# Kernel optimization log

Measured on AMD Instinct MI355X. Metric: run time of the kernel, lower is better.

Reference implementation:

```python
import jax, jax.numpy as jnp
import numpy as np

N, E, F, H, C = 100000, 1600000, 128, 128, 64

def setup_inputs() -> dict:
    key = jax.random.key(0)
    ks = jax.random.split(key, 16)
    def u(k, shape, fan_out):
        s = 1.0 / np.sqrt(fan_out)
        return jax.random.uniform(k, shape, jnp.float32, -s, s)
    return {
        'x': jax.random.normal(ks[0], (N, F), jnp.float32),
        'edge_index': jax.random.randint(ks[1], (2, E), 0, N, jnp.int32),
        # layer 1: F -> H  (stdv = 1/sqrt(out_features); att vecs stdv=1; att_vec stdv=1/sqrt(3))
        'W_low1': u(ks[2], (F, H), H), 'W_high1': u(ks[3], (F, H), H), 'W_mlp1': u(ks[4], (F, H), H),
        'v_low1': u(ks[5], (H, 1), 1), 'v_high1': u(ks[6], (H, 1), 1), 'v_mlp1': u(ks[7], (H, 1), 1),
        'att1': u(ks[8], (3, 3), 3),
        # layer 2: H -> C
        'W_low2': u(ks[9], (H, C), C), 'W_high2': u(ks[10], (H, C), C), 'W_mlp2': u(ks[11], (H, C), C),
        'v_low2': u(ks[12], (C, 1), 1), 'v_high2': u(ks[13], (C, 1), 1), 'v_mlp2': u(ks[14], (C, 1), 1),
        'att2': u(ks[15], (3, 3), 3),
    }

def reference(x, edge_index, W_low1, W_high1, W_mlp1, v_low1, v_high1, v_mlp1, att1,
              W_low2, W_high2, W_mlp2, v_low2, v_high2, v_mlp2, att2):
    row, col = edge_index[0], edge_index[1]
    # row-normalized adjacency: adj_low[i,j] = 1/deg(i); deg==0 rows -> zero output
    deg = jax.ops.segment_sum(jnp.ones((E,), x.dtype), row, num_segments=N)
    inv_deg = jnp.where(deg > 0, 1.0 / jnp.maximum(deg, 1.0), 0.0)[:, None]  # [N,1]

    def spmm_low(h):  # adj_low @ h
        return inv_deg * jax.ops.segment_sum(h[col], row, num_segments=N)

    T = 3.0
    def acm_layer(h, Wl, Wh, Wm, vl, vh, vm, av):
        hl = h @ Wl
        hh = h @ Wh
        out_low = jax.nn.relu(spmm_low(hl))
        out_high = jax.nn.relu(hh - spmm_low(hh))  # adj_high = I - adj_low
        out_mlp = jax.nn.relu(h @ Wm)
        logits = jnp.concatenate([out_low @ vl, out_high @ vh, out_mlp @ vm], axis=1)  # [N,3]
        att = jax.nn.softmax((jax.nn.sigmoid(logits) @ av) / T, axis=1)  # [N,3]
        return 3.0 * (att[:, 0:1] * out_low + att[:, 1:2] * out_high + att[:, 2:3] * out_mlp)

    fea = acm_layer(x, W_low1, W_high1, W_mlp1, v_low1, v_high1, v_mlp1, att1)
    fea = jax.nn.relu(fea)  # dropout is identity at eval
    return acm_layer(fea, W_low2, W_high2, W_mlp2, v_low2, v_high2, v_mlp2, att2)
```

## Files before the change

kernel.cpp:

```cpp
#include <hip/hip_runtime.h>

typedef unsigned short u16;
typedef unsigned int u32;
typedef unsigned long long u64;
typedef __attribute__((ext_vector_type(8))) short short8;
typedef __attribute__((ext_vector_type(4))) float f32x4;
typedef __attribute__((ext_vector_type(4))) u32 u32x4;

#define BSHIFT 8
#define MAXBUCK 512
#define BCAP 8192

__device__ __forceinline__ float bf2f(u32 u) {
    union { u32 i; float f; } v; v.i = u << 16; return v.f;
}
__device__ __forceinline__ float bf2fh(u32 u) {
    union { u32 i; float f; } v; v.i = u & 0xffff0000u; return v.f;
}
__device__ __forceinline__ u16 f2bf(float f) {
    union { float f; u32 i; } v; v.f = f;
    u32 u = (v.i + 0x7fffu + ((v.i >> 16) & 1u)) >> 16;
    return (u16)u;
}

__device__ __forceinline__ int swz(int ci) { return ci ^ ((ci >> 4) & 7); }

__device__ __forceinline__ int xcd_swz(int bid, int nbg) {
    int q = nbg >> 3, r = nbg & 7;
    int x = bid & 7, i = bid >> 3;
    return (x < r) ? (x * (q + 1) + i) : (r * (q + 1) + (x - r) * q + i);
}

#define CASTBLK 2048
__global__ void k_prep(const float4* __restrict__ X, u32* __restrict__ Xb, long total4,
                       const float* __restrict__ Wl1, const float* __restrict__ Wh1,
                       const float* __restrict__ Wm1, const float* __restrict__ Wl2,
                       const float* __restrict__ Wh2, const float* __restrict__ Wm2,
                       u16* __restrict__ Wp1, u16* __restrict__ Wp2) {
    if (blockIdx.x < CASTBLK) {
        long i = (long)blockIdx.x * blockDim.x + threadIdx.x;
        long stride = (long)CASTBLK * blockDim.x;
        for (; i < total4; i += stride) {
            float4 p = X[i];
            Xb[i * 2 + 0] = (u32)f2bf(p.x) | ((u32)f2bf(p.y) << 16);
            Xb[i * 2 + 1] = (u32)f2bf(p.z) | ((u32)f2bf(p.w) << 16);
        }
        return;
    }
    int tid = (blockIdx.x - CASTBLK) * blockDim.x + threadIdx.x;
    int nthr = 16 * blockDim.x;
    for (int m = 0; m < 8; ++m) {
        int layer = m >> 2;
        int slot = m & 3;
        int Hout = layer ? 64 : 128;
        const float* W = layer ? (slot == 0 ? Wl2 : (slot == 3 ? Wm2 : Wh2))
                               : (slot == 0 ? Wl1 : (slot == 3 ? Wm1 : Wh1));
        float sgn = (slot == 1) ? -1.f : 1.f;
        u16* dst = (layer ? Wp2 : Wp1) + slot * Hout * 128;
        int total = 128 * Hout;
        for (int i = tid; i < total; i += nthr) {
            int T = i / 2048;
            int c = (i / 512) & 3;
            int lane = (i / 8) & 63;
            int j = i & 7;
            int col = T * 16 + (lane & 15);
            int k = c * 32 + (lane >> 4) * 8 + j;
            dst[i] = f2bf(sgn * W[k * Hout + col]);
        }
    }
}

__global__ void k_bscatter_f(const int* __restrict__ erow, const int* __restrict__ ecol, int e,
                             int nbuck, int* __restrict__ gcursor, u32* __restrict__ bedge) {
    __shared__ int hist[MAXBUCK];
    __shared__ int base[MAXBUCK];
    for (int t = threadIdx.x; t < nbuck; t += blockDim.x) hist[t] = 0;
    __syncthreads();
    int chunk = (e + gridDim.x - 1) / gridDim.x;
    int lo = blockIdx.x * chunk, hi = min(e, lo + chunk);
    for (int i = lo + threadIdx.x; i < hi; i += blockDim.x)
        atomicAdd(&hist[erow[i] >> BSHIFT], 1);
    __syncthreads();
    for (int t = threadIdx.x; t < nbuck; t += blockDim.x) {
        int c = hist[t];
        base[t] = c ? atomicAdd(&gcursor[t], c) : 0;
        hist[t] = 0;
    }
    __syncthreads();
    for (int i = lo + threadIdx.x; i < hi; i += blockDim.x) {
        int r = erow[i];
        int bk = r >> BSHIFT;
        int pos = base[bk] + atomicAdd(&hist[bk], 1);
        if (pos < BCAP)
            bedge[(size_t)bk * BCAP + pos] = ((u32)ecol[i] << 8) | (u32)(r & 255);
    }
}

__global__ void k_bscan2(const int* __restrict__ bcnt, int nbuck, int* __restrict__ boff) {
    __shared__ int lds[MAXBUCK];
    int t = threadIdx.x;
    int v = (t < nbuck) ? bcnt[t] : 0;
    lds[t] = v; __syncthreads();
    for (int off = 1; off < MAXBUCK; off <<= 1) {
        int x = (t >= off) ? lds[t - off] : 0;
        __syncthreads();
        lds[t] += x;
        __syncthreads();
    }
    if (t < nbuck) {
        boff[t] = lds[t] - v;
        if (t == nbuck - 1) boff[nbuck] = lds[t];
    }
}

__global__ void k_bfill2f(const u32* __restrict__ bedge, const int* __restrict__ bcnt,
                          const int* __restrict__ boff, int n,
                          int* __restrict__ row_ptr, float* __restrict__ inv_deg,
                          int* __restrict__ cols) {
    __shared__ int cnt[256];
    __shared__ int incl[256];
    __shared__ int pos[256];
    int b = blockIdx.x, t = threadIdx.x;
    cnt[t] = 0;
    __syncthreads();
    int rbase = b << BSHIFT;
    const u32* src = bedge + (size_t)b * BCAP;
    int cb = bcnt[b];
    int lo = boff[b];
    for (int i = t; i < cb; i += 256)
        atomicAdd(&cnt[src[i] & 255u], 1);
    __syncthreads();
    int v = cnt[t];
    incl[t] = v;
    __syncthreads();
    for (int off = 1; off < 256; off <<= 1) {
        int x = (t >= off) ? incl[t - off] : 0;
        __syncthreads();
        incl[t] += x;
        __syncthreads();
    }
    int excl = incl[t] - v;
    pos[t] = excl;
    int row = rbase + t;
    if (row < n) {
        row_ptr[row] = lo + excl;
        inv_deg[row] = v > 0 ? 1.f / (float)v : 0.f;
    }
    if (b == (int)gridDim.x - 1 && t == 0) row_ptr[n] = lo + cb;
    __syncthreads();
    for (int i = t; i < cb; i += 256) {
        u32 vv = src[i];
        int rl = (int)(vv & 255u);
        int p = lo + atomicAdd(&pos[rl], 1);
        cols[p] = (int)(vv >> 8);
    }
}

template<int HOUT, bool L1>
__global__ __launch_bounds__(256, 4)
void k_fused(const u32* __restrict__ X2, const int* __restrict__ row_ptr,
             const int* __restrict__ cols, const float* __restrict__ inv_deg,
             const u16* __restrict__ Wp,
             const float* __restrict__ vl, const float* __restrict__ vh, const float* __restrict__ vm,
             const float* __restrict__ att, int n,
             u16* __restrict__ feaOut, float* __restrict__ fOut) {
    constexpr int KPG = HOUT / 64;
    constexpr int NTw = 3 * KPG;
    constexpr int ROWS = 16;
    __shared__ __align__(16) u32 AsU[1024];
    __shared__ __align__(16) u32 AxU[1024];
    __shared__ int rctr;
    int w = threadIdx.x >> 6, lane = threadIdx.x & 63;
    int ql = lane & 15;
    int ln15 = lane & 15, lq = lane >> 4;
    int tile = xcd_swz(blockIdx.x, gridDim.x);
    int m0 = tile * ROWS;
    const u32x4* X16 = (const u32x4*)X2;

    if (threadIdx.x == 0) rctr = 0;
    __syncthreads();

    for (;;) {
        int rv;
        if (ql == 0) rv = atomicAdd(&rctr, 1);
        rv = __shfl(rv, 0, 16);
        if (rv >= ROWS) break;
        int row = m0 + rv;
        int beg = 0, end = 0;
        float s = 0.f;
        u32x4 px = {0u, 0u, 0u, 0u};
        if (row < n) {
            beg = row_ptr[row];
            end = row_ptr[row + 1];
            s = inv_deg[row];
            px = X16[(size_t)row * 16 + ql];
        }
        float a0 = 0.f, a1 = 0.f, a2 = 0.f, a3 = 0.f, a4 = 0.f, a5 = 0.f, a6 = 0.f, a7 = 0.f;
        int myc = (beg + ql < end) ? cols[beg + ql] : 0;
        for (int j0 = beg; j0 < end; j0 += 16) {
            int cnt = end - j0; if (cnt > 16) cnt = 16;
            int nmy = (j0 + 16 + ql < end) ? cols[j0 + 16 + ql] : 0;
            int j = 0;
            for (; j + 8 <= cnt; j += 8) {
                int c0 = __shfl(myc, j + 0, 16);
                int c1 = __shfl(myc, j + 1, 16);
                int c2 = __shfl(myc, j + 2, 16);
                int c3 = __shfl(myc, j + 3, 16);
                int c4 = __shfl(myc, j + 4, 16);
                int c5 = __shfl(myc, j + 5, 16);
                int c6 = __shfl(myc, j + 6, 16);
                int c7 = __shfl(myc, j + 7, 16);
                u32x4 p0 = X16[(size_t)c0 * 16 + ql];
                u32x4 p1 = X16[(size_t)c1 * 16 + ql];
                u32x4 p2 = X16[(size_t)c2 * 16 + ql];
                u32x4 p3 = X16[(size_t)c3 * 16 + ql];
                u32x4 p4 = X16[(size_t)c4 * 16 + ql];
                u32x4 p5 = X16[(size_t)c5 * 16 + ql];
                u32x4 p6 = X16[(size_t)c6 * 16 + ql];
                u32x4 p7 = X16[(size_t)c7 * 16 + ql];
                a0 += bf2f(p0[0] & 0xffffu) + bf2f(p1[0] & 0xffffu) + bf2f(p2[0] & 0xffffu) + bf2f(p3[0] & 0xffffu)
                    + bf2f(p4[0] & 0xffffu) + bf2f(p5[0] & 0xffffu) + bf2f(p6[0] & 0xffffu) + bf2f(p7[0] & 0xffffu);
                a1 += bf2fh(p0[0]) + bf2fh(p1[0]) + bf2fh(p2[0]) + bf2fh(p3[0])
                    + bf2fh(p4[0]) + bf2fh(p5[0]) + bf2fh(p6[0]) + bf2fh(p7[0]);
                a2 += bf2f(p0[1] & 0xffffu) + bf2f(p1[1] & 0xffffu) + bf2f(p2[1] & 0xffffu) + bf2f(p3[1] & 0xffffu)
                    + bf2f(p4[1] & 0xffffu) + bf2f(p5[1] & 0xffffu) + bf2f(p6[1] & 0xffffu) + bf2f(p7[1] & 0xffffu);
                a3 += bf2fh(p0[1]) + bf2fh(p1[1]) + bf2fh(p2[1]) + bf2fh(p3[1])
                    + bf2fh(p4[1]) + bf2fh(p5[1]) + bf2fh(p6[1]) + bf2fh(p7[1]);
                a4 += bf2f(p0[2] & 0xffffu) + bf2f(p1[2] & 0xffffu) + bf2f(p2[2] & 0xffffu) + bf2f(p3[2] & 0xffffu)
                    + bf2f(p4[2] & 0xffffu) + bf2f(p5[2] & 0xffffu) + bf2f(p6[2] & 0xffffu) + bf2f(p7[2] & 0xffffu);
                a5 += bf2fh(p0[2]) + bf2fh(p1[2]) + bf2fh(p2[2]) + bf2fh(p3[2])
                    + bf2fh(p4[2]) + bf2fh(p5[2]) + bf2fh(p6[2]) + bf2fh(p7[2]);
                a6 += bf2f(p0[3] & 0xffffu) + bf2f(p1[3] & 0xffffu) + bf2f(p2[3] & 0xffffu) + bf2f(p3[3] & 0xffffu)
                    + bf2f(p4[3] & 0xffffu) + bf2f(p5[3] & 0xffffu) + bf2f(p6[3] & 0xffffu) + bf2f(p7[3] & 0xffffu);
                a7 += bf2fh(p0[3]) + bf2fh(p1[3]) + bf2fh(p2[3]) + bf2fh(p3[3])
                    + bf2fh(p4[3]) + bf2fh(p5[3]) + bf2fh(p6[3]) + bf2fh(p7[3]);
            }
            for (; j + 4 <= cnt; j += 4) {
                int c0 = __shfl(myc, j + 0, 16);
                int c1 = __shfl(myc, j + 1, 16);
                int c2 = __shfl(myc, j + 2, 16);
                int c3 = __shfl(myc, j + 3, 16);
                u32x4 p0 = X16[(size_t)c0 * 16 + ql];
                u32x4 p1 = X16[(size_t)c1 * 16 + ql];
                u32x4 p2 = X16[(size_t)c2 * 16 + ql];
                u32x4 p3 = X16[(size_t)c3 * 16 + ql];
                a0 += bf2f(p0[0] & 0xffffu) + bf2f(p1[0] & 0xffffu) + bf2f(p2[0] & 0xffffu) + bf2f(p3[0] & 0xffffu);
                a1 += bf2fh(p0[0]) + bf2fh(p1[0]) + bf2fh(p2[0]) + bf2fh(p3[0]);
                a2 += bf2f(p0[1] & 0xffffu) + bf2f(p1[1] & 0xffffu) + bf2f(p2[1] & 0xffffu) + bf2f(p3[1] & 0xffffu);
                a3 += bf2fh(p0[1]) + bf2fh(p1[1]) + bf2fh(p2[1]) + bf2fh(p3[1]);
                a4 += bf2f(p0[2] & 0xffffu) + bf2f(p1[2] & 0xffffu) + bf2f(p2[2] & 0xffffu) + bf2f(p3[2] & 0xffffu);
                a5 += bf2fh(p0[2]) + bf2fh(p1[2]) + bf2fh(p2[2]) + bf2fh(p3[2]);
                a6 += bf2f(p0[3] & 0xffffu) + bf2f(p1[3] & 0xffffu) + bf2f(p2[3] & 0xffffu) + bf2f(p3[3] & 0xffffu);
                a7 += bf2fh(p0[3]) + bf2fh(p1[3]) + bf2fh(p2[3]) + bf2fh(p3[3]);
            }
            for (; j < cnt; ++j) {
                int c = __shfl(myc, j, 16);
                u32x4 p = X16[(size_t)c * 16 + ql];
                a0 += bf2f(p[0] & 0xffffu);
                a1 += bf2fh(p[0]);
                a2 += bf2f(p[1] & 0xffffu);
                a3 += bf2fh(p[1]);
                a4 += bf2f(p[2] & 0xffffu);
                a5 += bf2fh(p[2]);
                a6 += bf2f(p[3] & 0xffffu);
                a7 += bf2fh(p[3]);
            }
            myc = nmy;
        }
        int ci = (ql >> 2) * 64 + (ql & 3) * 16 + rv;
        int d = swz(ci) * 4;
        u32x4 sv;
        sv[0] = (u32)f2bf(a0 * s) | ((u32)f2bf(a1 * s) << 16);
        sv[1] = (u32)f2bf(a2 * s) | ((u32)f2bf(a3 * s) << 16);
        sv[2] = (u32)f2bf(a4 * s) | ((u32)f2bf(a5 * s) << 16);
        sv[3] = (u32)f2bf(a6 * s) | ((u32)f2bf(a7 * s) << 16);
        *(u32x4*)(AsU + d) = sv;
        *(u32x4*)(AxU + d) = px;
    }

    f32x4 acc[NTw];
#pragma unroll
    for (int k = 0; k < NTw; ++k) { f32x4 z = {0.f, 0.f, 0.f, 0.f}; acc[k] = z; }

    __syncthreads();

    const u16* As = (const u16*)AsU;
    const u16* Ax = (const u16*)AxU;
#pragma unroll
    for (int c = 0; c < 4; ++c) {
        int ci = c * 64 + lane;
        int o = swz(ci) * 8;
        short8 as = *(const short8*)(As + o);
        short8 ax = *(const short8*)(Ax + o);
#pragma unroll
        for (int kk = 0; kk < KPG; ++kk) {
            int T = w + kk * 4;
            size_t fo = (size_t)(T * 4 + c) * 512 + lane * 8;
            short8 bl  = *(const short8*)(Wp + (size_t)0 * (HOUT * 128) + fo);
            short8 bhn = *(const short8*)(Wp + (size_t)1 * (HOUT * 128) + fo);
            short8 bhp = *(const short8*)(Wp + (size_t)2 * (HOUT * 128) + fo);
            short8 bm  = *(const short8*)(Wp + (size_t)3 * (HOUT * 128) + fo);
            acc[0 * KPG + kk] = __builtin_amdgcn_mfma_f32_16x16x32_bf16(as, bl,  acc[0 * KPG + kk], 0, 0, 0);
            acc[1 * KPG + kk] = __builtin_amdgcn_mfma_f32_16x16x32_bf16(as, bhn, acc[1 * KPG + kk], 0, 0, 0);
            acc[1 * KPG + kk] = __builtin_amdgcn_mfma_f32_16x16x32_bf16(ax, bhp, acc[1 * KPG + kk], 0, 0, 0);
            acc[2 * KPG + kk] = __builtin_amdgcn_mfma_f32_16x16x32_bf16(ax, bm,  acc[2 * KPG + kk], 0, 0, 0);
        }
    }

    float vval[NTw];
#pragma unroll
    for (int k = 0; k < NTw; ++k) {
        int g = k / KPG, kk = k % KPG;
        int col = w * 16 + kk * 64 + ln15;
        vval[k] = (g == 0 ? vl : (g == 1 ? vh : vm))[col];
    }

    __shared__ float part[4][3][ROWS];
    __shared__ float wgt[ROWS][3];
    {
        float pdg[3][4];
#pragma unroll
        for (int g = 0; g < 3; ++g)
#pragma unroll
            for (int r = 0; r < 4; ++r) pdg[g][r] = 0.f;
#pragma unroll
        for (int k = 0; k < NTw; ++k) {
            int g = k / KPG;
#pragma unroll
            for (int r = 0; r < 4; ++r)
                pdg[g][r] += fmaxf(acc[k][r], 0.f) * vval[k];
        }
#pragma unroll
        for (int off = 1; off < 16; off <<= 1)
#pragma unroll
            for (int g = 0; g < 3; ++g)
#pragma unroll
                for (int r = 0; r < 4; ++r)
                    pdg[g][r] += __shfl_xor(pdg[g][r], off);
        if (ln15 == 0) {
            int rbase = lq * 4;
#pragma unroll
            for (int g = 0; g < 3; ++g)
#pragma unroll
                for (int r = 0; r < 4; ++r)
                    part[w][g][rbase + r] = pdg[g][r];
        }
    }
    __syncthreads();
    if (threadIdx.x < ROWS) {
        int row = threadIdx.x;
        float d0 = 0.f, d1 = 0.f, d2 = 0.f;
#pragma unroll
        for (int q = 0; q < 4; ++q) {
            d0 += part[q][0][row];
            d1 += part[q][1][row];
            d2 += part[q][2][row];
        }
        float s0 = 1.f / (1.f + __expf(-d0));
        float s1 = 1.f / (1.f + __expf(-d1));
        float s2 = 1.f / (1.f + __expf(-d2));
        float a0 = (s0 * att[0] + s1 * att[3] + s2 * att[6]) * (1.f / 3.f);
        float a1 = (s0 * att[1] + s1 * att[4] + s2 * att[7]) * (1.f / 3.f);
        float a2 = (s0 * att[2] + s1 * att[5] + s2 * att[8]) * (1.f / 3.f);
        float mx = fmaxf(a0, fmaxf(a1, a2));
        float e0 = __expf(a0 - mx), e1 = __expf(a1 - mx), e2 = __expf(a2 - mx);
        float inv = 3.f / (e0 + e1 + e2);
        wgt[row][0] = e0 * inv;
        wgt[row][1] = e1 * inv;
        wgt[row][2] = e2 * inv;
    }
    __syncthreads();

#pragma unroll
    for (int kk = 0; kk < KPG; ++kk)
#pragma unroll
        for (int r = 0; r < 4; ++r) {
            int row_local = lq * 4 + r;
            int row = m0 + row_local;
            if (row < n) {
                int col = w * 16 + kk * 64 + ln15;
                float w0 = wgt[row_local][0], w1 = wgt[row_local][1], w2 = wgt[row_local][2];
                float ol = fmaxf(acc[0 * KPG + kk][r], 0.f);
                float oh = fmaxf(acc[1 * KPG + kk][r], 0.f);
                float om = fmaxf(acc[2 * KPG + kk][r], 0.f);
                float val = w0 * ol + w1 * oh + w2 * om;
                if (L1)
                    feaOut[(size_t)row * HOUT + col] = f2bf(fmaxf(val, 0.f));
                else
                    fOut[(size_t)row * HOUT + col] = val;
            }
        }
}

extern "C" void kernel_launch(void* const* d_in, const int* in_sizes, int n_in,
                              void* d_out, int out_size, void* d_ws, size_t ws_size,
                              hipStream_t stream) {
    const int F = 128;
    int n = in_sizes[0] / F;
    int e = in_sizes[1] / 2;
    int nbuck = (n + (1 << BSHIFT) - 1) >> BSHIFT;
    const float* x = (const float*)d_in[0];
    const int* ei = (const int*)d_in[1];
    const int* erow = ei;
    const int* ecol = ei + e;
    const float *Wl1 = (const float*)d_in[2], *Wh1 = (const float*)d_in[3], *Wm1 = (const float*)d_in[4];
    const float *vl1 = (const float*)d_in[5], *vh1 = (const float*)d_in[6], *vm1 = (const float*)d_in[7];
    const float* att1 = (const float*)d_in[8];
    const float *Wl2 = (const float*)d_in[9], *Wh2 = (const float*)d_in[10], *Wm2 = (const float*)d_in[11];
    const float *vl2 = (const float*)d_in[12], *vh2 = (const float*)d_in[13], *vm2 = (const float*)d_in[14];
    const float* att2 = (const float*)d_in[15];
    float* out = (float*)d_out;

    char* ws = (char*)d_ws;
    size_t off = 0;
    auto alloc = [&](size_t b) -> void* {
        void* p = ws + off;
        off = (off + b + 255) & ~(size_t)255;
        return p;
    };
    int* row_ptr = (int*)alloc((size_t)(n + 1) * 4);
    float* inv_deg = (float*)alloc((size_t)n * 4);
    int* gcursor = (int*)alloc(MAXBUCK * 4);
    int* boff = (int*)alloc((MAXBUCK + 1) * 4);
    u32* bedge = (u32*)alloc((size_t)MAXBUCK * BCAP * 4);
    int* cols = (int*)alloc((size_t)e * 4);
    u16* Xb = (u16*)alloc((size_t)n * 128 * 2);
    u16* fea = (u16*)alloc((size_t)n * 128 * 2);
    u16* Wp1 = (u16*)alloc((size_t)4 * 128 * 128 * 2);
    u16* Wp2 = (u16*)alloc((size_t)4 * 64 * 128 * 2);
    (void)ws_size; (void)n_in; (void)out_size;

    k_prep<<<CASTBLK + 16, 256, 0, stream>>>((const float4*)x, (u32*)Xb, (long)n * 32,
                                             Wl1, Wh1, Wm1, Wl2, Wh2, Wm2, Wp1, Wp2);

    hipMemsetAsync(gcursor, 0, (size_t)MAXBUCK * 4, stream);
    k_bscatter_f<<<256, 256, 0, stream>>>(erow, ecol, e, nbuck, gcursor, bedge);
    k_bscan2<<<1, MAXBUCK, 0, stream>>>(gcursor, nbuck, boff);
    k_bfill2f<<<nbuck, 256, 0, stream>>>(bedge, gcursor, boff, n, row_ptr, inv_deg, cols);

    int gb = (n + 15) / 16;

    k_fused<128, true><<<gb, 256, 0, stream>>>((const u32*)Xb, row_ptr, cols, inv_deg,
                                               Wp1, vl1, vh1, vm1, att1, n, fea, nullptr);
    k_fused<64, false><<<gb, 256, 0, stream>>>((const u32*)fea, row_ptr, cols, inv_deg,
                                               Wp2, vl2, vh2, vm2, att2, n, nullptr, out);
}
```

Measured before the change: 339.6 us.

## Make fused GNN layers persistent with atomic tile queue and merge prep kernels

The fused layer kernels become persistent: a capped grid of blocks pulls 16-row tiles from a global atomic counter instead of launching one block per tile with XCD swizzling. Attention parameters and v-vectors are hoisted out of the tile loop. Launch bounds rise to 6 blocks per CU. The input cast/weight-pack kernel and the edge bucket scatter kernel are merged into one launch. The aim is to cut launch and tail overhead and balance irregular row degrees, at the cost of per-tile atomics, extra barriers, the loss of XCD locality and more register pressure.

```diff
diff --git a/kernel.cpp b/kernel.cpp
--- a/kernel.cpp
+++ b/kernel.cpp
@@ -10,6 +10,8 @@
 #define BSHIFT 8
 #define MAXBUCK 512
 #define BCAP 8192
+#define CASTBLK 2048
+#define SCATBLK 256
 
 __device__ __forceinline__ float bf2f(u32 u) {
     union { u32 i; float f; } v; v.i = u << 16; return v.f;
@@ -25,18 +27,15 @@
 
 __device__ __forceinline__ int swz(int ci) { return ci ^ ((ci >> 4) & 7); }
 
-__device__ __forceinline__ int xcd_swz(int bid, int nbg) {
-    int q = nbg >> 3, r = nbg & 7;
-    int x = bid & 7, i = bid >> 3;
-    return (x < r) ? (x * (q + 1) + i) : (r * (q + 1) + (x - r) * q + i);
-}
-
-#define CASTBLK 2048
-__global__ void k_prep(const float4* __restrict__ X, u32* __restrict__ Xb, long total4,
-                       const float* __restrict__ Wl1, const float* __restrict__ Wh1,
-                       const float* __restrict__ Wm1, const float* __restrict__ Wl2,
-                       const float* __restrict__ Wh2, const float* __restrict__ Wm2,
-                       u16* __restrict__ Wp1, u16* __restrict__ Wp2) {
+__global__ void k_prep_scat(const float4* __restrict__ X, u32* __restrict__ Xb, long total4,
+                            const float* __restrict__ Wl1, const float* __restrict__ Wh1,
+                            const float* __restrict__ Wm1, const float* __restrict__ Wl2,
+                            const float* __restrict__ Wh2, const float* __restrict__ Wm2,
+                            u16* __restrict__ Wp1, u16* __restrict__ Wp2,
+                            const int* __restrict__ erow, const int* __restrict__ ecol, int e,
+                            int nbuck, int* __restrict__ gcursor, u32* __restrict__ bedge) {
+    __shared__ int hist[MAXBUCK];
+    __shared__ int base[MAXBUCK];
     if (blockIdx.x < CASTBLK) {
         long i = (long)blockIdx.x * blockDim.x + threadIdx.x;
         long stride = (long)CASTBLK * blockDim.x;
@@ -47,37 +46,35 @@
         }
         return;
     }
-    int tid = (blockIdx.x - CASTBLK) * blockDim.x + threadIdx.x;
-    int nthr = 16 * blockDim.x;
-    for (int m = 0; m < 8; ++m) {
-        int layer = m >> 2;
-        int slot = m & 3;
-        int Hout = layer ? 64 : 128;
-        const float* W = layer ? (slot == 0 ? Wl2 : (slot == 3 ? Wm2 : Wh2))
-                               : (slot == 0 ? Wl1 : (slot == 3 ? Wm1 : Wh1));
-        float sgn = (slot == 1) ? -1.f : 1.f;
-        u16* dst = (layer ? Wp2 : Wp1) + slot * Hout * 128;
-        int total = 128 * Hout;
-        for (int i = tid; i < total; i += nthr) {
-            int T = i / 2048;
-            int c = (i / 512) & 3;
-            int lane = (i / 8) & 63;
-            int j = i & 7;
-            int col = T * 16 + (lane & 15);
-            int k = c * 32 + (lane >> 4) * 8 + j;
-            dst[i] = f2bf(sgn * W[k * Hout + col]);
-        }
-    }
-}
-
-__global__ void k_bscatter_f(const int* __restrict__ erow, const int* __restrict__ ecol, int e,
-                             int nbuck, int* __restrict__ gcursor, u32* __restrict__ bedge) {
-    __shared__ int hist[MAXBUCK];
-    __shared__ int base[MAXBUCK];
+    if (blockIdx.x < CASTBLK + 16) {
+        int tid = (blockIdx.x - CASTBLK) * blockDim.x + threadIdx.x;
+        int nthr = 16 * blockDim.x;
+        for (int m = 0; m < 8; ++m) {
+            int layer = m >> 2;
+            int slot = m & 3;
+            int Hout = layer ? 64 : 128;
+            const float* W = layer ? (slot == 0 ? Wl2 : (slot == 3 ? Wm2 : Wh2))
+                                   : (slot == 0 ? Wl1 : (slot == 3 ? Wm1 : Wh1));
+            float sgn = (slot == 1) ? -1.f : 1.f;
+            u16* dst = (layer ? Wp2 : Wp1) + slot * Hout * 128;
+            int total = 128 * Hout;
+            for (int i = tid; i < total; i += nthr) {
+                int T = i / 2048;
+                int c = (i / 512) & 3;
+                int lane = (i / 8) & 63;
+                int j = i & 7;
+                int col = T * 16 + (lane & 15);
+                int k = c * 32 + (lane >> 4) * 8 + j;
+                dst[i] = f2bf(sgn * W[k * Hout + col]);
+            }
+        }
+        return;
+    }
+    int bid = blockIdx.x - (CASTBLK + 16);
     for (int t = threadIdx.x; t < nbuck; t += blockDim.x) hist[t] = 0;
     __syncthreads();
-    int chunk = (e + gridDim.x - 1) / gridDim.x;
-    int lo = blockIdx.x * chunk, hi = min(e, lo + chunk);
+    int chunk = (e + SCATBLK - 1) / SCATBLK;
+    int lo = bid * chunk, hi = min(e, lo + chunk);
     for (int i = lo + threadIdx.x; i < hi; i += blockDim.x)
         atomicAdd(&hist[erow[i] >> BSHIFT], 1);
     __syncthreads();
@@ -157,155 +154,26 @@
 }
 
 template<int HOUT, bool L1>
-__global__ __launch_bounds__(256, 4)
+__global__ __launch_bounds__(256, 6)
 void k_fused(const u32* __restrict__ X2, const int* __restrict__ row_ptr,
              const int* __restrict__ cols, const float* __restrict__ inv_deg,
              const u16* __restrict__ Wp,
              const float* __restrict__ vl, const float* __restrict__ vh, const float* __restrict__ vm,
-             const float* __restrict__ att, int n,
+             const float* __restrict__ att, int n, int ntiles, int* __restrict__ gctr,
              u16* __restrict__ feaOut, float* __restrict__ fOut) {
     constexpr int KPG = HOUT / 64;
     constexpr int NTw = 3 * KPG;
     constexpr int ROWS = 16;
     __shared__ __align__(16) u32 AsU[1024];
     __shared__ __align__(16) u32 AxU[1024];
+    __shared__ float part[4][3][ROWS];
+    __shared__ float wgt[ROWS][3];
+    __shared__ int tshare;
     __shared__ int rctr;
     int w = threadIdx.x >> 6, lane = threadIdx.x & 63;
     int ql = lane & 15;
     int ln15 = lane & 15, lq = lane >> 4;
-    int tile = xcd_swz(blockIdx.x, gridDim.x);
-    int m0 = tile * ROWS;
     const u32x4* X16 = (const u32x4*)X2;
-
-    if (threadIdx.x == 0) rctr = 0;
-    __syncthreads();
-
-    for (;;) {
-        int rv;
-        if (ql == 0) rv = atomicAdd(&rctr, 1);
-        rv = __shfl(rv, 0, 16);
-        if (rv >= ROWS) break;
-        int row = m0 + rv;
-        int beg = 0, end = 0;
-        float s = 0.f;
-        u32x4 px = {0u, 0u, 0u, 0u};
-        if (row < n) {
-            beg = row_ptr[row];
-            end = row_ptr[row + 1];
-            s = inv_deg[row];
-            px = X16[(size_t)row * 16 + ql];
-        }
-        float a0 = 0.f, a1 = 0.f, a2 = 0.f, a3 = 0.f, a4 = 0.f, a5 = 0.f, a6 = 0.f, a7 = 0.f;
-        int myc = (beg + ql < end) ? cols[beg + ql] : 0;
-        for (int j0 = beg; j0 < end; j0 += 16) {
-            int cnt = end - j0; if (cnt > 16) cnt = 16;
-            int nmy = (j0 + 16 + ql < end) ? cols[j0 + 16 + ql] : 0;
-            int j = 0;
-            for (; j + 8 <= cnt; j += 8) {
-                int c0 = __shfl(myc, j + 0, 16);
-                int c1 = __shfl(myc, j + 1, 16);
-                int c2 = __shfl(myc, j + 2, 16);
-                int c3 = __shfl(myc, j + 3, 16);
-                int c4 = __shfl(myc, j + 4, 16);
-                int c5 = __shfl(myc, j + 5, 16);
-                int c6 = __shfl(myc, j + 6, 16);
-                int c7 = __shfl(myc, j + 7, 16);
-                u32x4 p0 = X16[(size_t)c0 * 16 + ql];
-                u32x4 p1 = X16[(size_t)c1 * 16 + ql];
-                u32x4 p2 = X16[(size_t)c2 * 16 + ql];
-                u32x4 p3 = X16[(size_t)c3 * 16 + ql];
-                u32x4 p4 = X16[(size_t)c4 * 16 + ql];
-                u32x4 p5 = X16[(size_t)c5 * 16 + ql];
-                u32x4 p6 = X16[(size_t)c6 * 16 + ql];
-                u32x4 p7 = X16[(size_t)c7 * 16 + ql];
-                a0 += bf2f(p0[0] & 0xffffu) + bf2f(p1[0] & 0xffffu) + bf2f(p2[0] & 0xffffu) + bf2f(p3[0] & 0xffffu)
-                    + bf2f(p4[0] & 0xffffu) + bf2f(p5[0] & 0xffffu) + bf2f(p6[0] & 0xffffu) + bf2f(p7[0] & 0xffffu);
-                a1 += bf2fh(p0[0]) + bf2fh(p1[0]) + bf2fh(p2[0]) + bf2fh(p3[0])
-                    + bf2fh(p4[0]) + bf2fh(p5[0]) + bf2fh(p6[0]) + bf2fh(p7[0]);
-                a2 += bf2f(p0[1] & 0xffffu) + bf2f(p1[1] & 0xffffu) + bf2f(p2[1] & 0xffffu) + bf2f(p3[1] & 0xffffu)
-                    + bf2f(p4[1] & 0xffffu) + bf2f(p5[1] & 0xffffu) + bf2f(p6[1] & 0xffffu) + bf2f(p7[1] & 0xffffu);
-                a3 += bf2fh(p0[1]) + bf2fh(p1[1]) + bf2fh(p2[1]) + bf2fh(p3[1])
-                    + bf2fh(p4[1]) + bf2fh(p5[1]) + bf2fh(p6[1]) + bf2fh(p7[1]);
-                a4 += bf2f(p0[2] & 0xffffu) + bf2f(p1[2] & 0xffffu) + bf2f(p2[2] & 0xffffu) + bf2f(p3[2] & 0xffffu)
-                    + bf2f(p4[2] & 0xffffu) + bf2f(p5[2] & 0xffffu) + bf2f(p6[2] & 0xffffu) + bf2f(p7[2] & 0xffffu);
-                a5 += bf2fh(p0[2]) + bf2fh(p1[2]) + bf2fh(p2[2]) + bf2fh(p3[2])
-                    + bf2fh(p4[2]) + bf2fh(p5[2]) + bf2fh(p6[2]) + bf2fh(p7[2]);
-                a6 += bf2f(p0[3] & 0xffffu) + bf2f(p1[3] & 0xffffu) + bf2f(p2[3] & 0xffffu) + bf2f(p3[3] & 0xffffu)
-                    + bf2f(p4[3] & 0xffffu) + bf2f(p5[3] & 0xffffu) + bf2f(p6[3] & 0xffffu) + bf2f(p7[3] & 0xffffu);
-                a7 += bf2fh(p0[3]) + bf2fh(p1[3]) + bf2fh(p2[3]) + bf2fh(p3[3])
-                    + bf2fh(p4[3]) + bf2fh(p5[3]) + bf2fh(p6[3]) + bf2fh(p7[3]);
-            }
-            for (; j + 4 <= cnt; j += 4) {
-                int c0 = __shfl(myc, j + 0, 16);
-                int c1 = __shfl(myc, j + 1, 16);
-                int c2 = __shfl(myc, j + 2, 16);
-                int c3 = __shfl(myc, j + 3, 16);
-                u32x4 p0 = X16[(size_t)c0 * 16 + ql];
-                u32x4 p1 = X16[(size_t)c1 * 16 + ql];
-                u32x4 p2 = X16[(size_t)c2 * 16 + ql];
-                u32x4 p3 = X16[(size_t)c3 * 16 + ql];
-                a0 += bf2f(p0[0] & 0xffffu) + bf2f(p1[0] & 0xffffu) + bf2f(p2[0] & 0xffffu) + bf2f(p3[0] & 0xffffu);
-                a1 += bf2fh(p0[0]) + bf2fh(p1[0]) + bf2fh(p2[0]) + bf2fh(p3[0]);
-                a2 += bf2f(p0[1] & 0xffffu) + bf2f(p1[1] & 0xffffu) + bf2f(p2[1] & 0xffffu) + bf2f(p3[1] & 0xffffu);
-                a3 += bf2fh(p0[1]) + bf2fh(p1[1]) + bf2fh(p2[1]) + bf2fh(p3[1]);
-                a4 += bf2f(p0[2] & 0xffffu) + bf2f(p1[2] & 0xffffu) + bf2f(p2[2] & 0xffffu) + bf2f(p3[2] & 0xffffu);
-                a5 += bf2fh(p0[2]) + bf2fh(p1[2]) + bf2fh(p2[2]) + bf2fh(p3[2]);
-                a6 += bf2f(p0[3] & 0xffffu) + bf2f(p1[3] & 0xffffu) + bf2f(p2[3] & 0xffffu) + bf2f(p3[3] & 0xffffu);
-                a7 += bf2fh(p0[3]) + bf2fh(p1[3]) + bf2fh(p2[3]) + bf2fh(p3[3]);
-            }
-            for (; j < cnt; ++j) {
-                int c = __shfl(myc, j, 16);
-                u32x4 p = X16[(size_t)c * 16 + ql];
-                a0 += bf2f(p[0] & 0xffffu);
-                a1 += bf2fh(p[0]);
-                a2 += bf2f(p[1] & 0xffffu);
-                a3 += bf2fh(p[1]);
-                a4 += bf2f(p[2] & 0xffffu);
-                a5 += bf2fh(p[2]);
-                a6 += bf2f(p[3] & 0xffffu);
-                a7 += bf2fh(p[3]);
-            }
-            myc = nmy;
-        }
-        int ci = (ql >> 2) * 64 + (ql & 3) * 16 + rv;
-        int d = swz(ci) * 4;
-        u32x4 sv;
-        sv[0] = (u32)f2bf(a0 * s) | ((u32)f2bf(a1 * s) << 16);
-        sv[1] = (u32)f2bf(a2 * s) | ((u32)f2bf(a3 * s) << 16);
-        sv[2] = (u32)f2bf(a4 * s) | ((u32)f2bf(a5 * s) << 16);
-        sv[3] = (u32)f2bf(a6 * s) | ((u32)f2bf(a7 * s) << 16);
-        *(u32x4*)(AsU + d) = sv;
-        *(u32x4*)(AxU + d) = px;
-    }
-
-    f32x4 acc[NTw];
-#pragma unroll
-    for (int k = 0; k < NTw; ++k) { f32x4 z = {0.f, 0.f, 0.f, 0.f}; acc[k] = z; }
-
-    __syncthreads();
-
-    const u16* As = (const u16*)AsU;
-    const u16* Ax = (const u16*)AxU;
-#pragma unroll
-    for (int c = 0; c < 4; ++c) {
-        int ci = c * 64 + lane;
-        int o = swz(ci) * 8;
-        short8 as = *(const short8*)(As + o);
-        short8 ax = *(const short8*)(Ax + o);
-#pragma unroll
-        for (int kk = 0; kk < KPG; ++kk) {
-            int T = w + kk * 4;
-            size_t fo = (size_t)(T * 4 + c) * 512 + lane * 8;
-            short8 bl  = *(const short8*)(Wp + (size_t)0 * (HOUT * 128) + fo);
-            short8 bhn = *(const short8*)(Wp + (size_t)1 * (HOUT * 128) + fo);
-            short8 bhp = *(const short8*)(Wp + (size_t)2 * (HOUT * 128) + fo);
-            short8 bm  = *(const short8*)(Wp + (size_t)3 * (HOUT * 128) + fo);
-            acc[0 * KPG + kk] = __builtin_amdgcn_mfma_f32_16x16x32_bf16(as, bl,  acc[0 * KPG + kk], 0, 0, 0);
-            acc[1 * KPG + kk] = __builtin_amdgcn_mfma_f32_16x16x32_bf16(as, bhn, acc[1 * KPG + kk], 0, 0, 0);
-            acc[1 * KPG + kk] = __builtin_amdgcn_mfma_f32_16x16x32_bf16(ax, bhp, acc[1 * KPG + kk], 0, 0, 0);
-            acc[2 * KPG + kk] = __builtin_amdgcn_mfma_f32_16x16x32_bf16(ax, bm,  acc[2 * KPG + kk], 0, 0, 0);
-        }
-    }
 
     float vval[NTw];
 #pragma unroll
@@ -314,82 +182,221 @@
         int col = w * 16 + kk * 64 + ln15;
         vval[k] = (g == 0 ? vl : (g == 1 ? vh : vm))[col];
     }
-
-    __shared__ float part[4][3][ROWS];
-    __shared__ float wgt[ROWS][3];
-    {
-        float pdg[3][4];
-#pragma unroll
-        for (int g = 0; g < 3; ++g)
-#pragma unroll
-            for (int r = 0; r < 4; ++r) pdg[g][r] = 0.f;
-#pragma unroll
-        for (int k = 0; k < NTw; ++k) {
-            int g = k / KPG;
-#pragma unroll
-            for (int r = 0; r < 4; ++r)
-                pdg[g][r] += fmaxf(acc[k][r], 0.f) * vval[k];
-        }
-#pragma unroll
-        for (int off = 1; off < 16; off <<= 1)
+    float at0 = att[0], at1 = att[1], at2 = att[2], at3 = att[3], at4 = att[4];
+    float at5 = att[5], at6 = att[6], at7 = att[7], at8 = att[8];
+
+    for (;;) {
+        if (threadIdx.x == 0) {
+            tshare = atomicAdd(gctr, 1);
+            rctr = 0;
+        }
+        __syncthreads();
+        int tile = tshare;
+        if (tile >= ntiles) break;
+        int m0 = tile * ROWS;
+
+        for (;;) {
+            int rv;
+            if (ql == 0) rv = atomicAdd(&rctr, 1);
+            rv = __shfl(rv, 0, 16);
+            if (rv >= ROWS) break;
+            int row = m0 + rv;
+            int beg = 0, end = 0;
+            float s = 0.f;
+            u32x4 px = {0u, 0u, 0u, 0u};
+            if (row < n) {
+                beg = row_ptr[row];
+                end = row_ptr[row + 1];
+                s = inv_deg[row];
+                px = X16[(size_t)row * 16 + ql];
+            }
+            float a0 = 0.f, a1 = 0.f, a2 = 0.f, a3 = 0.f, a4 = 0.f, a5 = 0.f, a6 = 0.f, a7 = 0.f;
+            int myc = (beg + ql < end) ? cols[beg + ql] : 0;
+            for (int j0 = beg; j0 < end; j0 += 16) {
+                int cnt = end - j0; if (cnt > 16) cnt = 16;
+                int nmy = (j0 + 16 + ql < end) ? cols[j0 + 16 + ql] : 0;
+                int j = 0;
+                for (; j + 8 <= cnt; j += 8) {
+                    int c0 = __shfl(myc, j + 0, 16);
+                    int c1 = __shfl(myc, j + 1, 16);
+                    int c2 = __shfl(myc, j + 2, 16);
+                    int c3 = __shfl(myc, j + 3, 16);
+                    int c4 = __shfl(myc, j + 4, 16);
+                    int c5 = __shfl(myc, j + 5, 16);
+                    int c6 = __shfl(myc, j + 6, 16);
+                    int c7 = __shfl(myc, j + 7, 16);
+                    u32x4 p0 = X16[(size_t)c0 * 16 + ql];
+                    u32x4 p1 = X16[(size_t)c1 * 16 + ql];
+                    u32x4 p2 = X16[(size_t)c2 * 16 + ql];
+                    u32x4 p3 = X16[(size_t)c3 * 16 + ql];
+                    u32x4 p4 = X16[(size_t)c4 * 16 + ql];
+                    u32x4 p5 = X16[(size_t)c5 * 16 + ql];
+                    u32x4 p6 = X16[(size_t)c6 * 16 + ql];
+                    u32x4 p7 = X16[(size_t)c7 * 16 + ql];
+                    a0 += bf2f(p0[0] & 0xffffu) + bf2f(p1[0] & 0xffffu) + bf2f(p2[0] & 0xffffu) + bf2f(p3[0] & 0xffffu)
+                        + bf2f(p4[0] & 0xffffu) + bf2f(p5[0] & 0xffffu) + bf2f(p6[0] & 0xffffu) + bf2f(p7[0] & 0xffffu);
+                    a1 += bf2fh(p0[0]) + bf2fh(p1[0]) + bf2fh(p2[0]) + bf2fh(p3[0])
+                        + bf2fh(p4[0]) + bf2fh(p5[0]) + bf2fh(p6[0]) + bf2fh(p7[0]);
+                    a2 += bf2f(p0[1] & 0xffffu) + bf2f(p1[1] & 0xffffu) + bf2f(p2[1] & 0xffffu) + bf2f(p3[1] & 0xffffu)
+                        + bf2f(p4[1] & 0xffffu) + bf2f(p5[1] & 0xffffu) + bf2f(p6[1] & 0xffffu) + bf2f(p7[1] & 0xffffu);
+                    a3 += bf2fh(p0[1]) + bf2fh(p1[1]) + bf2fh(p2[1]) + bf2fh(p3[1])
+                        + bf2fh(p4[1]) + bf2fh(p5[1]) + bf2fh(p6[1]) + bf2fh(p7[1]);
+                    a4 += bf2f(p0[2] & 0xffffu) + bf2f(p1[2] & 0xffffu) + bf2f(p2[2] & 0xffffu) + bf2f(p3[2] & 0xffffu)
+                        + bf2f(p4[2] & 0xffffu) + bf2f(p5[2] & 0xffffu) + bf2f(p6[2] & 0xffffu) + bf2f(p7[2] & 0xffffu);
+                    a5 += bf2fh(p0[2]) + bf2fh(p1[2]) + bf2fh(p2[2]) + bf2fh(p3[2])
+                        + bf2fh(p4[2]) + bf2fh(p5[2]) + bf2fh(p6[2]) + bf2fh(p7[2]);
+                    a6 += bf2f(p0[3] & 0xffffu) + bf2f(p1[3] & 0xffffu) + bf2f(p2[3] & 0xffffu) + bf2f(p3[3] & 0xffffu)
+                        + bf2f(p4[3] & 0xffffu) + bf2f(p5[3] & 0xffffu) + bf2f(p6[3] & 0xffffu) + bf2f(p7[3] & 0xffffu);
+                    a7 += bf2fh(p0[3]) + bf2fh(p1[3]) + bf2fh(p2[3]) + bf2fh(p3[3])
+                        + bf2fh(p4[3]) + bf2fh(p5[3]) + bf2fh(p6[3]) + bf2fh(p7[3]);
+                }
+                for (; j + 4 <= cnt; j += 4) {
+                    int c0 = __shfl(myc, j + 0, 16);
+                    int c1 = __shfl(myc, j + 1, 16);
+                    int c2 = __shfl(myc, j + 2, 16);
+                    int c3 = __shfl(myc, j + 3, 16);
+                    u32x4 p0 = X16[(size_t)c0 * 16 + ql];
+                    u32x4 p1 = X16[(size_t)c1 * 16 + ql];
+                    u32x4 p2 = X16[(size_t)c2 * 16 + ql];
+                    u32x4 p3 = X16[(size_t)c3 * 16 + ql];
+                    a0 += bf2f(p0[0] & 0xffffu) + bf2f(p1[0] & 0xffffu) + bf2f(p2[0] & 0xffffu) + bf2f(p3[0] & 0xffffu);
+                    a1 += bf2fh(p0[0]) + bf2fh(p1[0]) + bf2fh(p2[0]) + bf2fh(p3[0]);
+                    a2 += bf2f(p0[1] & 0xffffu) + bf2f(p1[1] & 0xffffu) + bf2f(p2[1] & 0xffffu) + bf2f(p3[1] & 0xffffu);
+                    a3 += bf2fh(p0[1]) + bf2fh(p1[1]) + bf2fh(p2[1]) + bf2fh(p3[1]);
+                    a4 += bf2f(p0[2] & 0xffffu) + bf2f(p1[2] & 0xffffu) + bf2f(p2[2] & 0xffffu) + bf2f(p3[2] & 0xffffu);
+                    a5 += bf2fh(p0[2]) + bf2fh(p1[2]) + bf2fh(p2[2]) + bf2fh(p3[2]);
+                    a6 += bf2f(p0[3] & 0xffffu) + bf2f(p1[3] & 0xffffu) + bf2f(p2[3] & 0xffffu) + bf2f(p3[3] & 0xffffu);
+                    a7 += bf2fh(p0[3]) + bf2fh(p1[3]) + bf2fh(p2[3]) + bf2fh(p3[3]);
+                }
+                for (; j < cnt; ++j) {
+                    int c = __shfl(myc, j, 16);
+                    u32x4 p = X16[(size_t)c * 16 + ql];
+                    a0 += bf2f(p[0] & 0xffffu);
+                    a1 += bf2fh(p[0]);
+                    a2 += bf2f(p[1] & 0xffffu);
+                    a3 += bf2fh(p[1]);
+                    a4 += bf2f(p[2] & 0xffffu);
+                    a5 += bf2fh(p[2]);
+                    a6 += bf2f(p[3] & 0xffffu);
+                    a7 += bf2fh(p[3]);
+                }
+                myc = nmy;
+            }
+            int ci = (ql >> 2) * 64 + (ql & 3) * 16 + rv;
+            int d = swz(ci) * 4;
+            u32x4 sv;
+            sv[0] = (u32)f2bf(a0 * s) | ((u32)f2bf(a1 * s) << 16);
+            sv[1] = (u32)f2bf(a2 * s) | ((u32)f2bf(a3 * s) << 16);
+            sv[2] = (u32)f2bf(a4 * s) | ((u32)f2bf(a5 * s) << 16);
+            sv[3] = (u32)f2bf(a6 * s) | ((u32)f2bf(a7 * s) << 16);
+            *(u32x4*)(AsU + d) = sv;
+            *(u32x4*)(AxU + d) = px;
+        }
+
+        f32x4 acc[NTw];
+#pragma unroll
+        for (int k = 0; k < NTw; ++k) { f32x4 z = {0.f, 0.f, 0.f, 0.f}; acc[k] = z; }
+
+        __syncthreads();
+
+        const u16* As = (const u16*)AsU;
+        const u16* Ax = (const u16*)AxU;
+#pragma unroll
+        for (int c = 0; c < 4; ++c) {
+            int ci = c * 64 + lane;
+            int o = swz(ci) * 8;
+            short8 as = *(const short8*)(As + o);
+            short8 ax = *(const short8*)(Ax + o);
+#pragma unroll
+            for (int kk = 0; kk < KPG; ++kk) {
+                int T = w + kk * 4;
+                size_t fo = (size_t)(T * 4 + c) * 512 + lane * 8;
+                short8 bl  = *(const short8*)(Wp + (size_t)0 * (HOUT * 128) + fo);
+                short8 bhn = *(const short8*)(Wp + (size_t)1 * (HOUT * 128) + fo);
+                short8 bhp = *(const short8*)(Wp + (size_t)2 * (HOUT * 128) + fo);
+                short8 bm  = *(const short8*)(Wp + (size_t)3 * (HOUT * 128) + fo);
+                acc[0 * KPG + kk] = __builtin_amdgcn_mfma_f32_16x16x32_bf16(as, bl,  acc[0 * KPG + kk], 0, 0, 0);
+                acc[1 * KPG + kk] = __builtin_amdgcn_mfma_f32_16x16x32_bf16(as, bhn, acc[1 * KPG + kk], 0, 0, 0);
+                acc[1 * KPG + kk] = __builtin_amdgcn_mfma_f32_16x16x32_bf16(ax, bhp, acc[1 * KPG + kk], 0, 0, 0);
+                acc[2 * KPG + kk] = __builtin_amdgcn_mfma_f32_16x16x32_bf16(ax, bm,  acc[2 * KPG + kk], 0, 0, 0);
+            }
+        }
+
+        {
+            float pdg[3][4];
 #pragma unroll
             for (int g = 0; g < 3; ++g)
 #pragma unroll
+                for (int r = 0; r < 4; ++r) pdg[g][r] = 0.f;
+#pragma unroll
+            for (int k = 0; k < NTw; ++k) {
+                int g = k / KPG;
+#pragma unroll
                 for (int r = 0; r < 4; ++r)
-                    pdg[g][r] += __shfl_xor(pdg[g][r], off);
-        if (ln15 == 0) {
-            int rbase = lq * 4;
-#pragma unroll
-            for (int g = 0; g < 3; ++g)
-#pragma unroll
-                for (int r = 0; r < 4; ++r)
-                    part[w][g][rbase + r] = pdg[g][r];
-        }
-    }
-    __syncthreads();
-    if (threadIdx.x < ROWS) {
-        int row = threadIdx.x;
-        float d0 = 0.f, d1 = 0.f, d2 = 0.f;
-#pragma unroll
-        for (int q = 0; q < 4; ++q) {
-            d0 += part[q][0][row];
-            d1 += part[q][1][row];
-            d2 += part[q][2][row];
-        }
-        float s0 = 1.f / (1.f + __expf(-d0));
-        float s1 = 1.f / (1.f + __expf(-d1));
-        float s2 = 1.f / (1.f + __expf(-d2));
-        float a0 = (s0 * att[0] + s1 * att[3] + s2 * att[6]) * (1.f / 3.f);
-        float a1 = (s0 * att[1] + s1 * att[4] + s2 * att[7]) * (1.f / 3.f);
-        float a2 = (s0 * att[2] + s1 * att[5] + s2 * att[8]) * (1.f / 3.f);
-        float mx = fmaxf(a0, fmaxf(a1, a2));
-        float e0 = __expf(a0 - mx), e1 = __expf(a1 - mx), e2 = __expf(a2 - mx);
-        float inv = 3.f / (e0 + e1 + e2);
-        wgt[row][0] = e0 * inv;
-        wgt[row][1] = e1 * inv;
-        wgt[row][2] = e2 * inv;
-    }
-    __syncthreads();
-
-#pragma unroll
-    for (int kk = 0; kk < KPG; ++kk)
-#pragma unroll
-        for (int r = 0; r < 4; ++r) {
-            int row_local = lq * 4 + r;
-            int row = m0 + row_local;
-            if (row < n) {
-                int col = w * 16 + kk * 64 + ln15;
-                float w0 = wgt[row_local][0], w1 = wgt[row_local][1], w2 = wgt[row_local][2];
-                float ol = fmaxf(acc[0 * KPG + kk][r], 0.f);
-                float oh = fmaxf(acc[1 * KPG + kk][r], 0.f);
-                float om = fmaxf(acc[2 * KPG + kk][r], 0.f);
-                float val = w0 * ol + w1 * oh + w2 * om;
-                if (L1)
-                    feaOut[(size_t)row * HOUT + col] = f2bf(fmaxf(val, 0.f));
-                else
-                    fOut[(size_t)row * HOUT + col] = val;
-            }
-        }
+                    pdg[g][r] += fmaxf(acc[k][r], 0.f) * vval[k];
+            }
+#pragma unroll
+            for (int off = 1; off < 16; off <<= 1)
+#pragma unroll
+                for (int g = 0; g < 3; ++g)
+#pragma unroll
+                    for (int r = 0; r < 4; ++r)
+                        pdg[g][r] += __shfl_xor(pdg[g][r], off);
+            if (ln15 == 0) {
+                int rbase = lq * 4;
+#pragma unroll
+                for (int g = 0; g < 3; ++g)
+#pragma unroll
+                    for (int r = 0; r < 4; ++r)
+                        part[w][g][rbase + r] = pdg[g][r];
+            }
+        }
+        __syncthreads();
+        if (threadIdx.x < ROWS) {
+            int row = threadIdx.x;
+            float d0 = 0.f, d1 = 0.f, d2 = 0.f;
+#pragma unroll
+            for (int q = 0; q < 4; ++q) {
+                d0 += part[q][0][row];
+                d1 += part[q][1][row];
+                d2 += part[q][2][row];
+            }
+            float s0 = 1.f / (1.f + __expf(-d0));
+            float s1 = 1.f / (1.f + __expf(-d1));
+            float s2 = 1.f / (1.f + __expf(-d2));
+            float a0 = (s0 * at0 + s1 * at3 + s2 * at6) * (1.f / 3.f);
+            float a1 = (s0 * at1 + s1 * at4 + s2 * at7) * (1.f / 3.f);
+            float a2 = (s0 * at2 + s1 * at5 + s2 * at8) * (1.f / 3.f);
+            float mx = fmaxf(a0, fmaxf(a1, a2));
+            float e0 = __expf(a0 - mx), e1 = __expf(a1 - mx), e2 = __expf(a2 - mx);
+            float inv = 3.f / (e0 + e1 + e2);
+            wgt[row][0] = e0 * inv;
+            wgt[row][1] = e1 * inv;
+            wgt[row][2] = e2 * inv;
+        }
+        __syncthreads();
+
+#pragma unroll
+        for (int kk = 0; kk < KPG; ++kk)
+#pragma unroll
+            for (int r = 0; r < 4; ++r) {
+                int row_local = lq * 4 + r;
+                int row = m0 + row_local;
+                if (row < n) {
+                    int col = w * 16 + kk * 64 + ln15;
+                    float w0 = wgt[row_local][0], w1 = wgt[row_local][1], w2 = wgt[row_local][2];
+                    float ol = fmaxf(acc[0 * KPG + kk][r], 0.f);
+                    float oh = fmaxf(acc[1 * KPG + kk][r], 0.f);
+                    float om = fmaxf(acc[2 * KPG + kk][r], 0.f);
+                    float val = w0 * ol + w1 * oh + w2 * om;
+                    if (L1)
+                        feaOut[(size_t)row * HOUT + col] = f2bf(fmaxf(val, 0.f));
+                    else
+                        fOut[(size_t)row * HOUT + col] = val;
+                }
+            }
+        __syncthreads();
+    }
 }
 
 extern "C" void kernel_launch(void* const* d_in, const int* in_sizes, int n_in,
@@ -422,6 +429,7 @@
     float* inv_deg = (float*)alloc((size_t)n * 4);
     int* gcursor = (int*)alloc(MAXBUCK * 4);
     int* boff = (int*)alloc((MAXBUCK + 1) * 4);
+    int* gctr = (int*)alloc(2 * 4);
     u32* bedge = (u32*)alloc((size_t)MAXBUCK * BCAP * 4);
     int* cols = (int*)alloc((size_t)e * 4);
     u16* Xb = (u16*)alloc((size_t)n * 128 * 2);
@@ -430,18 +438,23 @@
     u16* Wp2 = (u16*)alloc((size_t)4 * 64 * 128 * 2);
     (void)ws_size; (void)n_in; (void)out_size;
 
-    k_prep<<<CASTBLK + 16, 256, 0, stream>>>((const float4*)x, (u32*)Xb, (long)n * 32,
-                                             Wl1, Wh1, Wm1, Wl2, Wh2, Wm2, Wp1, Wp2);
-
     hipMemsetAsync(gcursor, 0, (size_t)MAXBUCK * 4, stream);
-    k_bscatter_f<<<256, 256, 0, stream>>>(erow, ecol, e, nbuck, gcursor, bedge);
+    hipMemsetAsync(gctr, 0, 8, stream);
+
+    k_prep_scat<<<CASTBLK + 16 + SCATBLK, 256, 0, stream>>>(
+        (const float4*)x, (u32*)Xb, (long)n * 32,
+        Wl1, Wh1, Wm1, Wl2, Wh2, Wm2, Wp1, Wp2,
+        erow, ecol, e, nbuck, gcursor, bedge);
     k_bscan2<<<1, MAXBUCK, 0, stream>>>(gcursor, nbuck, boff);
     k_bfill2f<<<nbuck, 256, 0, stream>>>(bedge, gcursor, boff, n, row_ptr, inv_deg, cols);
 
-    int gb = (n + 15) / 16;
+    int ntiles = (n + 15) / 16;
+    int gb = ntiles < 1536 ? ntiles : 1536;
 
     k_fused<128, true><<<gb, 256, 0, stream>>>((const u32*)Xb, row_ptr, cols, inv_deg,
-                                               Wp1, vl1, vh1, vm1, att1, n, fea, nullptr);
+                                               Wp1, vl1, vh1, vm1, att1, n, ntiles, gctr + 0,
+                                               fea, nullptr);
     k_fused<64, false><<<gb, 256, 0, stream>>>((const u32*)fea, row_ptr, cols, inv_deg,
-                                               Wp2, vl2, vh2, vm2, att2, n, nullptr, out);
-}
+                                               Wp2, vl2, vh2, vm2, att2, n, ntiles, gctr + 1,
+                                               nullptr, out);
+}
```

New measurement: 525.1 us. +54.6%, slower.
